# Kernel tuning notes

Hardware: AMD Instinct MI355X
Metric: run time of the kernel (lower is better)

The kernel has to match this reference:

```python
import jax, jax.numpy as jnp
import numpy as np

D = 768      # num_hiddens (hardcoded by dense1/dense2/ln in the source)
H = 12       # num_heads
NEG = -1000000.0
EPS = 1e-5


def setup_inputs() -> dict:
    key = jax.random.key(0)
    ks = jax.random.split(key, 14)
    B, Lq, Lk = 8, 1024, 1024
    s = 0.02
    return {
        "queries": jax.random.normal(ks[0], (B, Lq, D), dtype=jnp.float32),
        "keys":    jax.random.normal(ks[1], (B, Lk, D), dtype=jnp.float32),
        "values":  jax.random.normal(ks[2], (B, Lk, D), dtype=jnp.float32),
        # binary padding masks; count_nonzero along axis 1 gives valid lens
        "mask_1": jax.random.randint(ks[3], (B, Lk), 0, 2, dtype=jnp.int32),
        "mask_2": jax.random.randint(ks[4], (B, Lq), 0, 2, dtype=jnp.int32),
        # projection weights stored as [in, out] (torch Linear is y = x @ W.T)
        "Wq": jax.random.normal(ks[5], (D, D), dtype=jnp.float32) * s,
        "Wk": jax.random.normal(ks[6], (D, D), dtype=jnp.float32) * s,
        "Wv": jax.random.normal(ks[7], (D, D), dtype=jnp.float32) * s,
        "Wo": jax.random.normal(ks[8], (D, D), dtype=jnp.float32) * s,
        "d1_w": jax.random.normal(ks[9], (D, D), dtype=jnp.float32) * s,
        "d1_b": jnp.zeros((D,), dtype=jnp.float32),
        "d2_w": jax.random.normal(ks[10], (D, D), dtype=jnp.float32) * s,
        "d2_b": jnp.zeros((D,), dtype=jnp.float32),
        "ln_g": jnp.ones((D,), dtype=jnp.float32),
        "ln_b": jnp.zeros((D,), dtype=jnp.float32),
    }


def _cross_att(queries, keys, values, mask_1, mask_2,
               Wq, Wk, Wv, Wo, d1_w, d1_b, d2_w, d2_b, ln_g, ln_b):
    B, Lq, _ = queries.shape
    Lk = keys.shape[1]
    hd = D // H
    # project + split heads: [B, H, L, hd]
    q = (queries @ Wq).reshape(B, Lq, H, hd).transpose(0, 2, 1, 3)
    k = (keys    @ Wk).reshape(B, Lk, H, hd).transpose(0, 2, 1, 3)
    v = (values  @ Wv).reshape(B, Lk, H, hd).transpose(0, 2, 1, 3)
    scores = jnp.einsum('bhqd,bhkd->bhqk', q, k) / jnp.sqrt(jnp.float32(hd))
    # dual-axis prefix mask from nonzero counts
    vl1 = jnp.sum(mask_1 != 0, axis=1)  # [B], masks key axis
    vl2 = jnp.sum(mask_2 != 0, axis=1)  # [B], masks query axis
    col_ok = jnp.arange(Lk)[None, None, None, :] < vl1[:, None, None, None]
    row_ok = jnp.arange(Lq)[None, None, :, None] < vl2[:, None, None, None]
    scores = jnp.where(col_ok & row_ok, scores, NEG)
    attn = jax.nn.softmax(scores, axis=-1)
    out = jnp.einsum('bhqk,bhkd->bhqd', attn, v)
    out = out.transpose(0, 2, 1, 3).reshape(B, Lq, D)
    mha = out @ Wo
    ffn = jax.nn.relu(mha @ d1_w + d1_b) @ d2_w + d2_b
    x = ffn + mha  # dropout is identity in eval
    mu = jnp.mean(x, axis=-1, keepdims=True)
    var = jnp.mean(jnp.square(x - mu), axis=-1, keepdims=True)
    return (x - mu) / jnp.sqrt(var + EPS) * ln_g + ln_b


def reference(queries, keys, values, mask_1, mask_2,
              Wq, Wk, Wv, Wo, d1_w, d1_b, d2_w, d2_b, ln_g, ln_b):
    return _cross_att(queries, keys, values, mask_1, mask_2,
                      Wq, Wk, Wv, Wo, d1_w, d1_b, d2_w, d2_b, ln_g, ln_b)
```

## Files before the change

### kernel.cpp

```cpp
#include <hip/hip_runtime.h>
#include <hip/hip_bf16.h>
#include <type_traits>

#define DM   768
#define NH   12
#define HD   64
#define BATCH 8
#define SEQ  1024
#define NROWS (BATCH * SEQ)

typedef short bf16x8 __attribute__((ext_vector_type(8)));
typedef float f32x4 __attribute__((ext_vector_type(4)));

__device__ inline unsigned short f2b(float x) {
    union { float f; unsigned int u; } v; v.f = x;
    return (unsigned short)((v.u + 0x8000u) >> 16);
}
__device__ inline unsigned int f2b2(float lo, float hi) {
    union { float f; unsigned int u; } a, b; a.f = lo; b.f = hi;
    return __builtin_amdgcn_perm(b.u + 0x8000u, a.u + 0x8000u, 0x07060302u);
}
__device__ inline float b2f(unsigned short u) {
    union { float f; unsigned int x; } v; v.x = ((unsigned int)u) << 16;
    return v.f;
}

__device__ inline void gld16(const unsigned short* g, unsigned short* l) {
    __builtin_amdgcn_global_load_lds(
        (const __attribute__((address_space(1))) unsigned int*)g,
        (__attribute__((address_space(3))) unsigned int*)l, 16, 0, 0);
}

__device__ __forceinline__ void mm2(const unsigned short* __restrict__ A,
                                    const unsigned short* __restrict__ Wt,
                                    int m0, int n0, int t,
                                    unsigned short (*As)[128][32],
                                    unsigned short (*Ws)[128][32],
                                    f32x4 (&acc)[4][4]) {
    const int w = t >> 6, lane = t & 63;
    const int quad = lane >> 4, l16 = lane & 15;
    const int wm = w & 1, wn = w >> 1;
    const int srow = 16 * w + (lane >> 2);
    const int scol = 8 * ((lane & 3) ^ ((lane >> 3) & 3));
    const int swr = (quad ^ ((l16 >> 1) & 3)) * 8;

#pragma unroll
    for (int i = 0; i < 4; ++i)
#pragma unroll
        for (int j = 0; j < 4; ++j) acc[i][j] = (f32x4){0.f, 0.f, 0.f, 0.f};

#pragma unroll
    for (int j = 0; j < 2; ++j) {
        gld16(&A[(size_t)(m0 + srow + 64 * j) * DM + scol], &As[0][16 * w + 64 * j][0]);
        gld16(&Wt[(size_t)(n0 + srow + 64 * j) * DM + scol], &Ws[0][16 * w + 64 * j][0]);
    }
    __syncthreads();

    for (int k0 = 0; k0 < DM; k0 += 32) {
        const int cur = (k0 >> 5) & 1;
        if (k0 + 32 < DM) {
#pragma unroll
            for (int j = 0; j < 2; ++j) {
                gld16(&A[(size_t)(m0 + srow + 64 * j) * DM + k0 + 32 + scol],
                      &As[cur ^ 1][16 * w + 64 * j][0]);
                gld16(&Wt[(size_t)(n0 + srow + 64 * j) * DM + k0 + 32 + scol],
                      &Ws[cur ^ 1][16 * w + 64 * j][0]);
            }
        }
        bf16x8 av[4], bv[4];
#pragma unroll
        for (int i = 0; i < 4; ++i)
            av[i] = *(const bf16x8*)&As[cur][wm * 64 + 16 * i + l16][swr];
#pragma unroll
        for (int i = 0; i < 4; ++i)
            bv[i] = *(const bf16x8*)&Ws[cur][wn * 64 + 16 * i + l16][swr];
#pragma unroll
        for (int i = 0; i < 4; ++i)
#pragma unroll
            for (int j = 0; j < 4; ++j)
                acc[i][j] = __builtin_amdgcn_mfma_f32_16x16x32_bf16(bv[j], av[i], acc[i][j], 0, 0, 0);
        __syncthreads();
    }
}

__global__ __launch_bounds__(256) void prep_kernel(const float* __restrict__ w0,
                                                   const float* __restrict__ w1,
                                                   const float* __restrict__ w2,
                                                   const float* __restrict__ w3,
                                                   const float* __restrict__ w4,
                                                   const float* __restrict__ w5,
                                                   unsigned short* __restrict__ wt,
                                                   unsigned short* __restrict__ wob,
                                                   const float* __restrict__ qin,
                                                   const float* __restrict__ kin,
                                                   const float* __restrict__ vin,
                                                   unsigned short* __restrict__ oq,
                                                   unsigned short* __restrict__ ok,
                                                   unsigned short* __restrict__ ov) {
    const int z = blockIdx.z;
    const int t = threadIdx.x;

    if (z < 4) {
        const int linear = z * 576 + blockIdx.y * 24 + blockIdx.x;
        const int c0 = linear * 4;
        const int g = c0 / 3072;
        const int r = c0 % 3072;
        const float* src = (g == 0) ? qin : (g == 1) ? kin : vin;
        unsigned short* dst = (g == 0) ? oq : (g == 1) ? ok : ov;
        const size_t i = ((size_t)r * 256 + t) * 8;
        float4 f[8];
#pragma unroll
        for (int c = 0; c < 4; ++c) {
            f[2 * c]     = ((const float4*)(src + i + (size_t)c * 2048))[0];
            f[2 * c + 1] = ((const float4*)(src + i + (size_t)c * 2048))[1];
        }
#pragma unroll
        for (int c = 0; c < 4; ++c) {
            uint4 p;
            p.x = f2b2(f[2 * c].x, f[2 * c].y);
            p.y = f2b2(f[2 * c].z, f[2 * c].w);
            p.z = f2b2(f[2 * c + 1].x, f[2 * c + 1].y);
            p.w = f2b2(f[2 * c + 1].z, f[2 * c + 1].w);
            *(uint4*)(dst + i + (size_t)c * 2048) = p;
        }
        return;
    }

    {
        __shared__ float tile[32][33];
        const int zz = z - 4;
        const float* W = (zz == 0) ? w0 : (zz == 1) ? w1 : (zz == 2) ? w2
                       : (zz == 3) ? w3 : (zz == 4) ? w4 : w5;
        unsigned short* Wt = wt + (size_t)zz * DM * DM;
        const int n0 = blockIdx.x * 32;
        const int k0 = blockIdx.y * 32;
        const int tx = t & 31;
        const int ty = t >> 5;
        float v[4];
#pragma unroll
        for (int r = 0; r < 4; ++r) {
            v[r] = W[(size_t)(k0 + ty + 8 * r) * DM + n0 + tx];
            tile[ty + 8 * r][tx] = v[r];
        }
        if (zz == 3) {
#pragma unroll
            for (int r = 0; r < 4; ++r)
                wob[(size_t)(k0 + ty + 8 * r) * DM + n0 + tx] = f2b(v[r]);
        }
        __syncthreads();
#pragma unroll
        for (int r = 0; r < 4; ++r)
            Wt[(size_t)(n0 + ty + 8 * r) * DM + k0 + tx] = f2b(tile[tx][ty + 8 * r]);
    }
}

__global__ __launch_bounds__(256) void qkv_gemm(const unsigned short* __restrict__ aq,
                                                const unsigned short* __restrict__ akk,
                                                const unsigned short* __restrict__ av_,
                                                unsigned short* __restrict__ wt,
                                                const unsigned short* __restrict__ wob,
                                                unsigned short* __restrict__ c0,
                                                unsigned short* __restrict__ c1,
                                                unsigned short* __restrict__ c2,
                                                const int* __restrict__ m1,
                                                const int* __restrict__ m2,
                                                int* __restrict__ lens,
                                                float* __restrict__ vp) {
    __shared__ __align__(16) unsigned short As[2][128][32];
    __shared__ __align__(16) unsigned short Ws[2][128][32];

    const int t = threadIdx.x;
    const size_t WT = (size_t)DM * DM;

    const unsigned short* A;
    const unsigned short* Wop;
    unsigned short* C;
    float cs = 1.0f;
    int m0, n0, g = -1;

    if (blockIdx.y == 0) {
        if (blockIdx.x >= 52) return;
        if (blockIdx.x >= 36) {
            const int bid = blockIdx.x - 36;
            int* redi = (int*)&As[0][0][0];
            const int b = bid & 7;
            const int* m = (bid < 8) ? m1 : m2;
            int cnt = 0;
            for (int i = t; i < SEQ; i += 256) cnt += (m[b * SEQ + i] != 0) ? 1 : 0;
            redi[t] = cnt;
            __syncthreads();
            for (int off = 128; off > 0; off >>= 1) {
                if (t < off) redi[t] += redi[t + off];
                __syncthreads();
            }
            if (t == 0) lens[bid] = redi[0];
            return;
        }
        A = wt + 4 * WT;
        Wop = wob;
        C = wt + 6 * WT;
        m0 = (blockIdx.x % 6) * 128;
        n0 = (blockIdx.x / 6) * 128;
    } else {
        const int yy = blockIdx.y - 1;
        g = yy / 6;
        m0 = blockIdx.x * 128;
        n0 = (yy % 6) * 128;
        A = (g == 0) ? aq : (g == 1) ? akk : av_;
        Wop = wt + (size_t)g * WT;
        C = (g == 0) ? c0 : (g == 1) ? c1 : c2;
        cs = (g == 0) ? 0.18033688f : 1.0f;
    }

    f32x4 acc[4][4];
    mm2(A, Wop, m0, n0, t, As, Ws, acc);

    const int w = t >> 6, lane = t & 63;
    const int quad = lane >> 4, l16 = lane & 15;
    const int wm = w & 1, wn = w >> 1;

#pragma unroll
    for (int i = 0; i < 4; ++i) {
        const int tok = m0 + wm * 64 + 16 * i + l16;
        unsigned short* crow = &C[(size_t)tok * DM + n0 + wn * 64 + quad * 4];
#pragma unroll
        for (int j = 0; j < 4; ++j) {
            uint2 pr;
            pr.x = f2b2(acc[i][j][0] * cs, acc[i][j][1] * cs);
            pr.y = f2b2(acc[i][j][2] * cs, acc[i][j][3] * cs);
            *(uint2*)(crow + 16 * j) = pr;
        }
    }

    if (g == 2) {
        float s2[4][4];
#pragma unroll
        for (int j = 0; j < 4; ++j)
#pragma unroll
            for (int r = 0; r < 4; ++r) {
                float sv = acc[0][j][r] + acc[1][j][r] + acc[2][j][r] + acc[3][j][r];
#pragma unroll
                for (int d = 1; d < 16; d <<= 1) sv += __shfl_xor(sv, d, 64);
                s2[j][r] = sv;
            }
        float mine = 0.f;
#pragma unroll
        for (int j = 0; j < 4; ++j)
#pragma unroll
            for (int r = 0; r < 4; ++r)
                if ((l16 >> 2) == j && (l16 & 3) == r) mine = s2[j][r];
        float* sc = (float*)&As[0][0][0];
        const int slot = (wn * 4 + quad) * 16 + l16;
        __syncthreads();
        if (wm == 1) sc[slot] = mine;
        __syncthreads();
        if (wm == 0) {
            const int col = n0 + wn * 64 + 16 * (l16 >> 2) + quad * 4 + (l16 & 3);
            const int bb = m0 >> 10;
            const int chunk = (m0 >> 7) & 7;
            const int hh = col >> 6;
            vp[((size_t)(bb * NH + hh) * 8 + chunk) * 64 + (col & 63)] = mine + sc[slot];
        }
    }
}

template <typename CT>
__global__ __launch_bounds__(256) void gemm_bf(const unsigned short* __restrict__ A,
                                               const unsigned short* __restrict__ Wt,
                                               CT* __restrict__ C,
                                               const float* __restrict__ bias,
                                               const unsigned short* __restrict__ res,
                                               int relu) {
    __shared__ __align__(16) unsigned short As[2][128][32];
    __shared__ __align__(16) unsigned short Ws[2][128][32];

    const int t = threadIdx.x;
    const int m0 = blockIdx.x * 128;
    const int n0 = blockIdx.y * 128;

    f32x4 acc[4][4];
    mm2(A, Wt, m0, n0, t, As, Ws, acc);

    const int w = t >> 6, lane = t & 63;
    const int quad = lane >> 4, l16 = lane & 15;
    const int wm = w & 1, wn = w >> 1;

#pragma unroll
    for (int i = 0; i < 4; ++i) {
        const int tok = m0 + wm * 64 + 16 * i + l16;
#pragma unroll
        for (int j = 0; j < 4; ++j) {
            const int fb = n0 + wn * 64 + 16 * j + quad * 4;
            float cv0 = acc[i][j][0], cv1 = acc[i][j][1];
            float cv2 = acc[i][j][2], cv3 = acc[i][j][3];
            if (bias) {
                const float4 bb = *(const float4*)&bias[fb];
                cv0 += bb.x; cv1 += bb.y; cv2 += bb.z; cv3 += bb.w;
            }
            if (relu) {
                cv0 = fmaxf(cv0, 0.0f); cv1 = fmaxf(cv1, 0.0f);
                cv2 = fmaxf(cv2, 0.0f); cv3 = fmaxf(cv3, 0.0f);
            }
            if (res) {
                const uint2 rr = *(const uint2*)&res[(size_t)tok * DM + fb];
                cv0 += b2f((unsigned short)(rr.x & 0xffffu));
                cv1 += b2f((unsigned short)(rr.x >> 16));
                cv2 += b2f((unsigned short)(rr.y & 0xffffu));
                cv3 += b2f((unsigned short)(rr.y >> 16));
            }
            if constexpr (std::is_same<CT, float>::value) {
                float4 o4; o4.x = cv0; o4.y = cv1; o4.z = cv2; o4.w = cv3;
                *(float4*)&C[(size_t)tok * DM + fb] = o4;
            } else {
                uint2 pr;
                pr.x = f2b2(cv0, cv1);
                pr.y = f2b2(cv2, cv3);
                *(uint2*)&C[(size_t)tok * DM + fb] = pr;
            }
        }
    }
}

__global__ __launch_bounds__(256) void gemm_mh(const unsigned short* __restrict__ A,
                                               const unsigned short* __restrict__ wt,
                                               unsigned short* __restrict__ cm,
                                               unsigned short* __restrict__ ch,
                                               const float* __restrict__ d1b) {
    __shared__ __align__(16) unsigned short As[2][128][32];
    __shared__ __align__(16) unsigned short Ws[2][128][32];

    const int t = threadIdx.x;
    const int unit = blockIdx.y / 6;
    const unsigned short* Wt = wt + (size_t)(unit ? 6 : 3) * DM * DM;
    unsigned short* C = unit ? ch : cm;
    const int m0 = blockIdx.x * 128;
    const int n0 = (blockIdx.y % 6) * 128;

    f32x4 acc[4][4];
    mm2(A, Wt, m0, n0, t, As, Ws, acc);

    const int w = t >> 6, lane = t & 63;
    const int quad = lane >> 4, l16 = lane & 15;
    const int wm = w & 1, wn = w >> 1;

#pragma unroll
    for (int i = 0; i < 4; ++i) {
        const int tok = m0 + wm * 64 + 16 * i + l16;
#pragma unroll
        for (int j = 0; j < 4; ++j) {
            const int fb = n0 + wn * 64 + 16 * j + quad * 4;
            float cv0 = acc[i][j][0], cv1 = acc[i][j][1];
            float cv2 = acc[i][j][2], cv3 = acc[i][j][3];
            if (unit) {
                const float4 bb = *(const float4*)&d1b[fb];
                cv0 = fmaxf(cv0 + bb.x, 0.0f);
                cv1 = fmaxf(cv1 + bb.y, 0.0f);
                cv2 = fmaxf(cv2 + bb.z, 0.0f);
                cv3 = fmaxf(cv3 + bb.w, 0.0f);
            }
            uint2 pr;
            pr.x = f2b2(cv0, cv1);
            pr.y = f2b2(cv2, cv3);
            *(uint2*)&C[(size_t)tok * DM + fb] = pr;
        }
    }
}

__global__ __launch_bounds__(256) void attn_mfma(const unsigned short* Q,
                                                 const unsigned short* __restrict__ K,
                                                 const unsigned short* __restrict__ V,
                                                 unsigned short* O,
                                                 const int* __restrict__ lens,
                                                 const float* __restrict__ vp) {
    __shared__ __align__(16) unsigned short Ks[64][72];
    __shared__ __align__(16) unsigned short Vt[64][72];
    __shared__ __align__(16) unsigned short Ps[4][16][72];

    const int t = threadIdx.x;
    const int bid = blockIdx.x;
    const int q0 = (bid & 15) * 64;
    const int h = (bid >> 4) % NH;
    const int b = bid / (16 * NH);
    const int vl1 = lens[b];
    const int vl2 = lens[8 + b];
    const int wid = t >> 6;
    const int lane = t & 63;
    const int quad = lane >> 4;
    const int l16 = lane & 15;
    const size_t vpb = (size_t)(b * NH + h) * 8 * 64;

    if (q0 >= vl2 || vl1 == 0) {
        float vm[4];
#pragma unroll
        for (int ct = 0; ct < 4; ++ct) {
            float s = 0.0f;
#pragma unroll
            for (int c = 0; c < 8; ++c) s += vp[vpb + (size_t)c * 64 + 16 * ct + l16];
            vm[ct] = s * (1.0f / 1024.0f);
        }
#pragma unroll
        for (int r = 0; r < 4; ++r) {
            const size_t row = (size_t)(b * SEQ + q0 + 16 * wid + quad * 4 + r);
#pragma unroll
            for (int ct = 0; ct < 4; ++ct)
                O[row * DM + h * HD + 16 * ct + l16] = f2b(vm[ct]);
        }
        return;
    }

    bf16x8 qa0, qa1;
    {
        const unsigned short* qp =
            &Q[(size_t)(b * SEQ + q0 + 16 * wid + l16) * DM + h * HD + quad * 8];
        qa0 = *(const bf16x8*)qp;
        qa1 = *(const bf16x8*)(qp + 32);
    }

    f32x4 o[4];
#pragma unroll
    for (int ct = 0; ct < 4; ++ct) o[ct] = (f32x4){0.f, 0.f, 0.f, 0.f};
    float suml[4];
    bool rbad[4];
#pragma unroll
    for (int r = 0; r < 4; ++r) {
        suml[r] = 0.0f;
        rbad[r] = (q0 + 16 * wid + quad * 4 + r) >= vl2;
    }

    const int nt = (vl1 + 63) >> 6;

    const int kkr = t >> 3;
    const int khc = (t & 7) * 8;
    const unsigned short* kbase = &K[(size_t)(b * SEQ) * DM + h * HD];
    const unsigned short* vbase = &V[(size_t)(b * SEQ) * DM + h * HD];

    uint4 kr0 = *(const uint4*)&kbase[(size_t)kkr * DM + khc];
    uint4 kr1 = *(const uint4*)&kbase[(size_t)(kkr + 32) * DM + khc];
    uint4 vr0 = *(const uint4*)&vbase[(size_t)lane * DM + wid * 16];
    uint4 vr1 = *(const uint4*)&vbase[(size_t)lane * DM + wid * 16 + 8];

    const int k2 = l16 >> 2;

    for (int tile = 0; tile < nt; ++tile) {
        const int c0 = tile * 64;
        *(uint4*)&Ks[kkr][khc] = kr0;
        *(uint4*)&Ks[kkr + 32][khc] = kr1;
        {
            union { uint4 u; unsigned short s[8]; } va, vb;
            va.u = vr0; vb.u = vr1;
#pragma unroll
            for (int j = 0; j < 8; ++j) Vt[wid * 16 + j][lane] = va.s[j];
#pragma unroll
            for (int j = 0; j < 8; ++j) Vt[wid * 16 + 8 + j][lane] = vb.s[j];
        }
        __syncthreads();

        if (tile < nt - 1) {
            const int c1 = c0 + 64;
            kr0 = *(const uint4*)&kbase[(size_t)(c1 + kkr) * DM + khc];
            kr1 = *(const uint4*)&kbase[(size_t)(c1 + kkr + 32) * DM + khc];
            vr0 = *(const uint4*)&vbase[(size_t)(c1 + lane) * DM + wid * 16];
            vr1 = *(const uint4*)&vbase[(size_t)(c1 + lane) * DM + wid * 16 + 8];
        }

        f32x4 s[4];
        __builtin_amdgcn_s_setprio(1);
#pragma unroll
        for (int ct = 0; ct < 4; ++ct) {
            f32x4 acc = (f32x4){0.f, 0.f, 0.f, 0.f};
            bf16x8 b0v = *(const bf16x8*)&Ks[16 * ct + l16][quad * 8];
            bf16x8 b1v = *(const bf16x8*)&Ks[16 * ct + l16][32 + quad * 8];
            acc = __builtin_amdgcn_mfma_f32_16x16x32_bf16(qa0, b0v, acc, 0, 0, 0);
            acc = __builtin_amdgcn_mfma_f32_16x16x32_bf16(qa1, b1v, acc, 0, 0, 0);
            s[ct] = acc;
        }
        __builtin_amdgcn_s_setprio(0);
#pragma unroll
        for (int ct = 0; ct < 4; ++ct) {
            const bool kok = (c0 + 16 * ct + l16) < vl1;
#pragma unroll
            for (int r = 0; r < 4; ++r) {
                float e = __builtin_amdgcn_exp2f(s[ct][r]);
                float p = kok ? e : 0.0f;
                s[ct][r] = p;
                suml[r] += p;
            }
        }
#pragma unroll
        for (int ct = 0; ct < 4; ++ct) {
            const int gidx = 2 * ct + (l16 >> 3);
            const int c = l16 & 7;
            const int gs = (gidx ^ quad) * 8 + c;
#pragma unroll
            for (int r = 0; r < 4; ++r)
                Ps[wid][quad * 4 + r][gs] = f2b(s[ct][r]);
        }
        bf16x8 pa0 = *(const bf16x8*)&Ps[wid][l16][(quad ^ k2) * 8];
        bf16x8 pa1 = *(const bf16x8*)&Ps[wid][l16][((4 + quad) ^ k2) * 8];
        __builtin_amdgcn_s_setprio(1);
#pragma unroll
        for (int ct = 0; ct < 4; ++ct) {
            bf16x8 vb0 = *(const bf16x8*)&Vt[16 * ct + l16][quad * 8];
            bf16x8 vb1 = *(const bf16x8*)&Vt[16 * ct + l16][32 + quad * 8];
            o[ct] = __builtin_amdgcn_mfma_f32_16x16x32_bf16(pa0, vb0, o[ct], 0, 0, 0);
            o[ct] = __builtin_amdgcn_mfma_f32_16x16x32_bf16(pa1, vb1, o[ct], 0, 0, 0);
        }
        __builtin_amdgcn_s_setprio(0);
        __syncthreads();
    }

#pragma unroll
    for (int d = 1; d < 16; d <<= 1) {
#pragma unroll
        for (int r = 0; r < 4; ++r) suml[r] += __shfl_xor(suml[r], d, 64);
    }

    float vm[4];
    if (rbad[0] || rbad[3]) {
#pragma unroll
        for (int ct = 0; ct < 4; ++ct) {
            float s = 0.0f;
#pragma unroll
            for (int c = 0; c < 8; ++c) s += vp[vpb + (size_t)c * 64 + 16 * ct + l16];
            vm[ct] = s * (1.0f / 1024.0f);
        }
    }
#pragma unroll
    for (int r = 0; r < 4; ++r) {
        const float inv = 1.0f / suml[r];
        const size_t row = (size_t)(b * SEQ + q0 + 16 * wid + quad * 4 + r);
#pragma unroll
        for (int ct = 0; ct < 4; ++ct) {
            const float val = rbad[r] ? vm[ct] : o[ct][r] * inv;
            O[row * DM + h * HD + 16 * ct + l16] = f2b(val);
        }
    }
}

__global__ __launch_bounds__(256) void ln_kernel(float* __restrict__ X,
                                                 const float* __restrict__ g,
                                                 const float* __restrict__ bvec) {
    __shared__ float red[256];
    const int row = blockIdx.x;
    const int t = threadIdx.x;
    float* xr = X + (size_t)row * DM;
    float4 x = make_float4(0.f, 0.f, 0.f, 0.f);
    if (t < 192) x = *(const float4*)&xr[t * 4];
    red[t] = x.x + x.y + x.z + x.w;
    __syncthreads();
    for (int off = 128; off > 0; off >>= 1) {
        if (t < off) red[t] += red[t + off];
        __syncthreads();
    }
    float mu = red[0] * (1.0f / 768.0f);
    __syncthreads();
    float d0 = 0.f, d1 = 0.f, d2 = 0.f, d3 = 0.f;
    if (t < 192) { d0 = x.x - mu; d1 = x.y - mu; d2 = x.z - mu; d3 = x.w - mu; }
    red[t] = d0 * d0 + d1 * d1 + d2 * d2 + d3 * d3;
    __syncthreads();
    for (int off = 128; off > 0; off >>= 1) {
        if (t < off) red[t] += red[t + off];
        __syncthreads();
    }
    float rstd = rsqrtf(red[0] * (1.0f / 768.0f) + 1e-5f);
    if (t < 192) {
        const float4 gg = *(const float4*)&g[t * 4];
        const float4 bb = *(const float4*)&bvec[t * 4];
        float4 o4;
        o4.x = d0 * rstd * gg.x + bb.x;
        o4.y = d1 * rstd * gg.y + bb.y;
        o4.z = d2 * rstd * gg.z + bb.z;
        o4.w = d3 * rstd * gg.w + bb.w;
        *(float4*)&xr[t * 4] = o4;
    }
}

extern "C" void kernel_launch(void* const* d_in, const int* in_sizes, int n_in,
                              void* d_out, int out_size, void* d_ws, size_t ws_size,
                              hipStream_t stream) {
    const float* queries = (const float*)d_in[0];
    const float* keys    = (const float*)d_in[1];
    const float* values  = (const float*)d_in[2];
    const int* mask1 = (const int*)d_in[3];
    const int* mask2 = (const int*)d_in[4];
    const float* Wq  = (const float*)d_in[5];
    const float* Wk  = (const float*)d_in[6];
    const float* Wv  = (const float*)d_in[7];
    const float* Wo  = (const float*)d_in[8];
    const float* d1w = (const float*)d_in[9];
    const float* d1b = (const float*)d_in[10];
    const float* d2w = (const float*)d_in[11];
    const float* d2b = (const float*)d_in[12];
    const float* lng = (const float*)d_in[13];
    const float* lnb = (const float*)d_in[14];

    char* ws = (char*)d_ws;
    int* lens = (int*)ws;
    float* vp = (float*)(ws + 256);
    const size_t VP = (size_t)96 * 8 * 64 * sizeof(float);
    const size_t NB = (size_t)NROWS * DM * sizeof(unsigned short);
    const size_t WT = (size_t)DM * DM;
    unsigned short* b0 = (unsigned short*)(ws + 256 + VP);
    unsigned short* b1 = (unsigned short*)(ws + 256 + VP + NB);
    unsigned short* b2 = (unsigned short*)(ws + 256 + VP + 2 * NB);
    unsigned short* wt = (unsigned short*)(ws + 256 + VP + 3 * NB);
    unsigned short* aq = (unsigned short*)(ws + 256 + VP + 3 * NB + 7 * WT * sizeof(unsigned short));
    unsigned short* ak = aq + (size_t)NROWS * DM;
    unsigned short* av = ak + (size_t)NROWS * DM;
    unsigned short* wob = av + (size_t)NROWS * DM;
    float* xout = (float*)d_out;

    prep_kernel<<<dim3(24, 24, 10), 256, 0, stream>>>(Wq, Wk, Wv, Wo, d1w, d2w,
                                                      wt, wob, queries, keys, values,
                                                      aq, ak, av);

    qkv_gemm<<<dim3(64, 19), 256, 0, stream>>>(aq, ak, av, wt, wob, b0, b1, b2,
                                               mask1, mask2, lens, vp);

    attn_mfma<<<16 * NH * BATCH, 256, 0, stream>>>(b0, b1, b2, b0, lens, vp);

    gemm_mh<<<dim3(64, 12), 256, 0, stream>>>(b0, wt, b1, b2, d1b);

    gemm_bf<float><<<dim3(64, 6), 256, 0, stream>>>(b2, wt + 5 * WT, xout, d2b, b1, 0);

    ln_kernel<<<NROWS, 256, 0, stream>>>(xout, lng, lnb);
}
```

Baseline: 301.9 us.

## Fuse fp32-to-bf16 activation conversion into QKV GEMM tile loads

Removes the separate pass that converted queries/keys/values to bf16 in prep_kernel. The QKV GEMM now streams fp32 activations straight into LDS with swizzled global_load_lds and converts to bf16 while building MFMA operands. This saves writing and re-reading three bf16 activation copies, at the cost of twice the LDS traffic for the A tiles and extra conversion ALU work inside the GEMM loop. It also removes the setprio hints in attention and rewrites layernorm to use scalar strided accesses with all 256 threads instead of float4 on 192 threads.

```diff
diff --git a/kernel.cpp b/kernel.cpp
--- a/kernel.cpp
+++ b/kernel.cpp
@@ -26,6 +26,11 @@
 }
 
 __device__ inline void gld16(const unsigned short* g, unsigned short* l) {
+    __builtin_amdgcn_global_load_lds(
+        (const __attribute__((address_space(1))) unsigned int*)g,
+        (__attribute__((address_space(3))) unsigned int*)l, 16, 0, 0);
+}
+__device__ inline void gld16f(const float* g, float* l) {
     __builtin_amdgcn_global_load_lds(
         (const __attribute__((address_space(1))) unsigned int*)g,
         (__attribute__((address_space(3))) unsigned int*)l, 16, 0, 0);
@@ -83,6 +88,69 @@
     }
 }
 
+__device__ __forceinline__ void mm2f(const float* __restrict__ Af,
+                                     const unsigned short* __restrict__ Wt,
+                                     int m0, int n0, int t,
+                                     float (*As)[128][32],
+                                     unsigned short (*Ws)[128][32],
+                                     f32x4 (&acc)[4][4]) {
+    const int w = t >> 6, lane = t & 63;
+    const int quad = lane >> 4, l16 = lane & 15;
+    const int wm = w & 1, wn = w >> 1;
+    const int srow = 16 * w + (lane >> 2);
+    const int scol = 8 * ((lane & 3) ^ ((lane >> 3) & 3));
+    const int swr = (quad ^ ((l16 >> 1) & 3)) * 8;
+    const int ar = lane >> 3;
+    const int as_ = lane & 7;
+
+#pragma unroll
+    for (int i = 0; i < 4; ++i)
+#pragma unroll
+        for (int j = 0; j < 4; ++j) acc[i][j] = (f32x4){0.f, 0.f, 0.f, 0.f};
+
+    auto stage = [&](int k0, int b) {
+#pragma unroll
+        for (int j = 0; j < 4; ++j) {
+            const int row = 32 * j + 8 * w + ar;
+            gld16f(&Af[(size_t)(m0 + row) * DM + k0 + ((as_ ^ ar) << 2)],
+                   &As[b][32 * j + 8 * w][0]);
+        }
+#pragma unroll
+        for (int j = 0; j < 2; ++j)
+            gld16(&Wt[(size_t)(n0 + srow + 64 * j) * DM + k0 + scol],
+                  &Ws[b][16 * w + 64 * j][0]);
+    };
+
+    stage(0, 0);
+    __syncthreads();
+
+    for (int k0 = 0; k0 < DM; k0 += 32) {
+        const int cur = (k0 >> 5) & 1;
+        if (k0 + 32 < DM) stage(k0 + 32, cur ^ 1);
+        bf16x8 av[4], bv[4];
+#pragma unroll
+        for (int i = 0; i < 4; ++i) {
+            const int rx = wm * 64 + 16 * i + l16;
+            const int hx = l16 & 7;
+            const float4 f0 = *(const float4*)&As[cur][rx][((2 * quad) ^ hx) << 2];
+            const float4 f1 = *(const float4*)&As[cur][rx][((2 * quad + 1) ^ hx) << 2];
+            union { unsigned int u[4]; bf16x8 v; } cv;
+            cv.u[0] = f2b2(f0.x, f0.y); cv.u[1] = f2b2(f0.z, f0.w);
+            cv.u[2] = f2b2(f1.x, f1.y); cv.u[3] = f2b2(f1.z, f1.w);
+            av[i] = cv.v;
+        }
+#pragma unroll
+        for (int i = 0; i < 4; ++i)
+            bv[i] = *(const bf16x8*)&Ws[cur][wn * 64 + 16 * i + l16][swr];
+#pragma unroll
+        for (int i = 0; i < 4; ++i)
+#pragma unroll
+            for (int j = 0; j < 4; ++j)
+                acc[i][j] = __builtin_amdgcn_mfma_f32_16x16x32_bf16(bv[j], av[i], acc[i][j], 0, 0, 0);
+        __syncthreads();
+    }
+}
+
 __global__ __launch_bounds__(256) void prep_kernel(const float* __restrict__ w0,
                                                    const float* __restrict__ w1,
                                                    const float* __restrict__ w2,
@@ -90,73 +158,37 @@
                                                    const float* __restrict__ w4,
                                                    const float* __restrict__ w5,
                                                    unsigned short* __restrict__ wt,
-                                                   unsigned short* __restrict__ wob,
-                                                   const float* __restrict__ qin,
-                                                   const float* __restrict__ kin,
-                                                   const float* __restrict__ vin,
-                                                   unsigned short* __restrict__ oq,
-                                                   unsigned short* __restrict__ ok,
-                                                   unsigned short* __restrict__ ov) {
+                                                   unsigned short* __restrict__ wob) {
     const int z = blockIdx.z;
     const int t = threadIdx.x;
-
-    if (z < 4) {
-        const int linear = z * 576 + blockIdx.y * 24 + blockIdx.x;
-        const int c0 = linear * 4;
-        const int g = c0 / 3072;
-        const int r = c0 % 3072;
-        const float* src = (g == 0) ? qin : (g == 1) ? kin : vin;
-        unsigned short* dst = (g == 0) ? oq : (g == 1) ? ok : ov;
-        const size_t i = ((size_t)r * 256 + t) * 8;
-        float4 f[8];
-#pragma unroll
-        for (int c = 0; c < 4; ++c) {
-            f[2 * c]     = ((const float4*)(src + i + (size_t)c * 2048))[0];
-            f[2 * c + 1] = ((const float4*)(src + i + (size_t)c * 2048))[1];
-        }
-#pragma unroll
-        for (int c = 0; c < 4; ++c) {
-            uint4 p;
-            p.x = f2b2(f[2 * c].x, f[2 * c].y);
-            p.y = f2b2(f[2 * c].z, f[2 * c].w);
-            p.z = f2b2(f[2 * c + 1].x, f[2 * c + 1].y);
-            p.w = f2b2(f[2 * c + 1].z, f[2 * c + 1].w);
-            *(uint4*)(dst + i + (size_t)c * 2048) = p;
-        }
-        return;
-    }
-
-    {
-        __shared__ float tile[32][33];
-        const int zz = z - 4;
-        const float* W = (zz == 0) ? w0 : (zz == 1) ? w1 : (zz == 2) ? w2
-                       : (zz == 3) ? w3 : (zz == 4) ? w4 : w5;
-        unsigned short* Wt = wt + (size_t)zz * DM * DM;
-        const int n0 = blockIdx.x * 32;
-        const int k0 = blockIdx.y * 32;
-        const int tx = t & 31;
-        const int ty = t >> 5;
-        float v[4];
-#pragma unroll
-        for (int r = 0; r < 4; ++r) {
-            v[r] = W[(size_t)(k0 + ty + 8 * r) * DM + n0 + tx];
-            tile[ty + 8 * r][tx] = v[r];
-        }
-        if (zz == 3) {
-#pragma unroll
-            for (int r = 0; r < 4; ++r)
-                wob[(size_t)(k0 + ty + 8 * r) * DM + n0 + tx] = f2b(v[r]);
-        }
-        __syncthreads();
+    __shared__ float tile[32][33];
+    const float* W = (z == 0) ? w0 : (z == 1) ? w1 : (z == 2) ? w2
+                   : (z == 3) ? w3 : (z == 4) ? w4 : w5;
+    unsigned short* Wt = wt + (size_t)z * DM * DM;
+    const int n0 = blockIdx.x * 32;
+    const int k0 = blockIdx.y * 32;
+    const int tx = t & 31;
+    const int ty = t >> 5;
+    float v[4];
+#pragma unroll
+    for (int r = 0; r < 4; ++r) {
+        v[r] = W[(size_t)(k0 + ty + 8 * r) * DM + n0 + tx];
+        tile[ty + 8 * r][tx] = v[r];
+    }
+    if (z == 3) {
 #pragma unroll
         for (int r = 0; r < 4; ++r)
-            Wt[(size_t)(n0 + ty + 8 * r) * DM + k0 + tx] = f2b(tile[tx][ty + 8 * r]);
-    }
-}
-
-__global__ __launch_bounds__(256) void qkv_gemm(const unsigned short* __restrict__ aq,
-                                                const unsigned short* __restrict__ akk,
-                                                const unsigned short* __restrict__ av_,
+            wob[(size_t)(k0 + ty + 8 * r) * DM + n0 + tx] = f2b(v[r]);
+    }
+    __syncthreads();
+#pragma unroll
+    for (int r = 0; r < 4; ++r)
+        Wt[(size_t)(n0 + ty + 8 * r) * DM + k0 + tx] = f2b(tile[tx][ty + 8 * r]);
+}
+
+__global__ __launch_bounds__(256) void qkv_gemm(const float* __restrict__ qin,
+                                                const float* __restrict__ kin,
+                                                const float* __restrict__ vin,
                                                 unsigned short* __restrict__ wt,
                                                 const unsigned short* __restrict__ wob,
                                                 unsigned short* __restrict__ c0,
@@ -166,14 +198,13 @@
                                                 const int* __restrict__ m2,
                                                 int* __restrict__ lens,
                                                 float* __restrict__ vp) {
-    __shared__ __align__(16) unsigned short As[2][128][32];
-    __shared__ __align__(16) unsigned short Ws[2][128][32];
+    __shared__ __align__(16) float Asf[2][128][32];
+    __shared__ __align__(16) unsigned short Wsb[2][128][32];
 
     const int t = threadIdx.x;
     const size_t WT = (size_t)DM * DM;
 
-    const unsigned short* A;
-    const unsigned short* Wop;
+    f32x4 acc[4][4];
     unsigned short* C;
     float cs = 1.0f;
     int m0, n0, g = -1;
@@ -182,7 +213,7 @@
         if (blockIdx.x >= 52) return;
         if (blockIdx.x >= 36) {
             const int bid = blockIdx.x - 36;
-            int* redi = (int*)&As[0][0][0];
+            int* redi = (int*)&Asf[0][0][0];
             const int b = bid & 7;
             const int* m = (bid < 8) ? m1 : m2;
             int cnt = 0;
@@ -196,24 +227,21 @@
             if (t == 0) lens[bid] = redi[0];
             return;
         }
-        A = wt + 4 * WT;
-        Wop = wob;
-        C = wt + 6 * WT;
         m0 = (blockIdx.x % 6) * 128;
         n0 = (blockIdx.x / 6) * 128;
+        C = wt + 6 * WT;
+        mm2(wt + 4 * WT, wob, m0, n0, t,
+            (unsigned short (*)[128][32])&Asf[0][0][0], Wsb, acc);
     } else {
         const int yy = blockIdx.y - 1;
         g = yy / 6;
         m0 = blockIdx.x * 128;
         n0 = (yy % 6) * 128;
-        A = (g == 0) ? aq : (g == 1) ? akk : av_;
-        Wop = wt + (size_t)g * WT;
+        const float* Af = (g == 0) ? qin : (g == 1) ? kin : vin;
         C = (g == 0) ? c0 : (g == 1) ? c1 : c2;
         cs = (g == 0) ? 0.18033688f : 1.0f;
-    }
-
-    f32x4 acc[4][4];
-    mm2(A, Wop, m0, n0, t, As, Ws, acc);
+        mm2f(Af, wt + (size_t)g * WT, m0, n0, t, Asf, Wsb, acc);
+    }
 
     const int w = t >> 6, lane = t & 63;
     const int quad = lane >> 4, l16 = lane & 15;
@@ -249,7 +277,7 @@
 #pragma unroll
             for (int r = 0; r < 4; ++r)
                 if ((l16 >> 2) == j && (l16 & 3) == r) mine = s2[j][r];
-        float* sc = (float*)&As[0][0][0];
+        float* sc = (float*)&Asf[0][0][0];
         const int slot = (wn * 4 + quad) * 16 + l16;
         __syncthreads();
         if (wm == 1) sc[slot] = mine;
@@ -464,7 +492,6 @@
         }
 
         f32x4 s[4];
-        __builtin_amdgcn_s_setprio(1);
 #pragma unroll
         for (int ct = 0; ct < 4; ++ct) {
             f32x4 acc = (f32x4){0.f, 0.f, 0.f, 0.f};
@@ -474,7 +501,6 @@
             acc = __builtin_amdgcn_mfma_f32_16x16x32_bf16(qa1, b1v, acc, 0, 0, 0);
             s[ct] = acc;
         }
-        __builtin_amdgcn_s_setprio(0);
 #pragma unroll
         for (int ct = 0; ct < 4; ++ct) {
             const bool kok = (c0 + 16 * ct + l16) < vl1;
@@ -497,7 +523,6 @@
         }
         bf16x8 pa0 = *(const bf16x8*)&Ps[wid][l16][(quad ^ k2) * 8];
         bf16x8 pa1 = *(const bf16x8*)&Ps[wid][l16][((4 + quad) ^ k2) * 8];
-        __builtin_amdgcn_s_setprio(1);
 #pragma unroll
         for (int ct = 0; ct < 4; ++ct) {
             bf16x8 vb0 = *(const bf16x8*)&Vt[16 * ct + l16][quad * 8];
@@ -505,7 +530,6 @@
             o[ct] = __builtin_amdgcn_mfma_f32_16x16x32_bf16(pa0, vb0, o[ct], 0, 0, 0);
             o[ct] = __builtin_amdgcn_mfma_f32_16x16x32_bf16(pa1, vb1, o[ct], 0, 0, 0);
         }
-        __builtin_amdgcn_s_setprio(0);
         __syncthreads();
     }
 
@@ -544,9 +568,10 @@
     const int row = blockIdx.x;
     const int t = threadIdx.x;
     float* xr = X + (size_t)row * DM;
-    float4 x = make_float4(0.f, 0.f, 0.f, 0.f);
-    if (t < 192) x = *(const float4*)&xr[t * 4];
-    red[t] = x.x + x.y + x.z + x.w;
+    float x0 = xr[t];
+    float x1 = xr[t + 256];
+    float x2 = xr[t + 512];
+    red[t] = x0 + x1 + x2;
     __syncthreads();
     for (int off = 128; off > 0; off >>= 1) {
         if (t < off) red[t] += red[t + off];
@@ -554,25 +579,17 @@
     }
     float mu = red[0] * (1.0f / 768.0f);
     __syncthreads();
-    float d0 = 0.f, d1 = 0.f, d2 = 0.f, d3 = 0.f;
-    if (t < 192) { d0 = x.x - mu; d1 = x.y - mu; d2 = x.z - mu; d3 = x.w - mu; }
-    red[t] = d0 * d0 + d1 * d1 + d2 * d2 + d3 * d3;
+    float d0 = x0 - mu, d1 = x1 - mu, d2 = x2 - mu;
+    red[t] = d0 * d0 + d1 * d1 + d2 * d2;
     __syncthreads();
     for (int off = 128; off > 0; off >>= 1) {
         if (t < off) red[t] += red[t + off];
         __syncthreads();
     }
     float rstd = rsqrtf(red[0] * (1.0f / 768.0f) + 1e-5f);
-    if (t < 192) {
-        const float4 gg = *(const float4*)&g[t * 4];
-        const float4 bb = *(const float4*)&bvec[t * 4];
-        float4 o4;
-        o4.x = d0 * rstd * gg.x + bb.x;
-        o4.y = d1 * rstd * gg.y + bb.y;
-        o4.z = d2 * rstd * gg.z + bb.z;
-        o4.w = d3 * rstd * gg.w + bb.w;
-        *(float4*)&xr[t * 4] = o4;
-    }
+    xr[t]       = d0 * rstd * g[t]       + bvec[t];
+    xr[t + 256] = d1 * rstd * g[t + 256] + bvec[t + 256];
+    xr[t + 512] = d2 * rstd * g[t + 512] + bvec[t + 512];
 }
 
 extern "C" void kernel_launch(void* const* d_in, const int* in_sizes, int n_in,
@@ -604,18 +621,14 @@
     unsigned short* b1 = (unsigned short*)(ws + 256 + VP + NB);
     unsigned short* b2 = (unsigned short*)(ws + 256 + VP + 2 * NB);
     unsigned short* wt = (unsigned short*)(ws + 256 + VP + 3 * NB);
-    unsigned short* aq = (unsigned short*)(ws + 256 + VP + 3 * NB + 7 * WT * sizeof(unsigned short));
-    unsigned short* ak = aq + (size_t)NROWS * DM;
-    unsigned short* av = ak + (size_t)NROWS * DM;
-    unsigned short* wob = av + (size_t)NROWS * DM;
+    unsigned short* wob = wt + 7 * WT;
     float* xout = (float*)d_out;
 
-    prep_kernel<<<dim3(24, 24, 10), 256, 0, stream>>>(Wq, Wk, Wv, Wo, d1w, d2w,
-                                                      wt, wob, queries, keys, values,
-                                                      aq, ak, av);
-
-    qkv_gemm<<<dim3(64, 19), 256, 0, stream>>>(aq, ak, av, wt, wob, b0, b1, b2,
-                                               mask1, mask2, lens, vp);
+    prep_kernel<<<dim3(24, 24, 6), 256, 0, stream>>>(Wq, Wk, Wv, Wo, d1w, d2w,
+                                                     wt, wob);
+
+    qkv_gemm<<<dim3(64, 19), 256, 0, stream>>>(queries, keys, values, wt, wob,
+                                               b0, b1, b2, mask1, mask2, lens, vp);
 
     attn_mfma<<<16 * NH * BATCH, 256, 0, stream>>>(b0, b1, b2, b0, lens, vp);
 
```

Result: no change. 304.6 us (+0.9%).
